# Kernel optimization log

Measured on AMD Instinct MI355X. Metric: run time of the kernel, lower is better.

## Reference

```python
import jax, jax.numpy as jnp
import numpy as np

N_QUBITS = 10
N_LAYERS = 2
B = 4096
D_IN = 512
D_OUT = 256


def _apply_1q(state, gate, wire, n):
    # state: (B, 2**n) complex64; gate: (2,2) shared or (B,2,2) batched
    b = state.shape[0]
    left, right = 2 ** wire, 2 ** (n - wire - 1)
    s = state.reshape(b, left, 2, right)
    if gate.ndim == 3:
        s = jnp.einsum('bij,bljr->blir', gate, s)
    else:
        s = jnp.einsum('ij,bljr->blir', gate, s)
    return s.reshape(b, 2 ** n)


def _apply_cnot(state, c, t, n):
    # CNOT(control=c, target=t): flip target axis on the control=1 slice
    b = state.shape[0]
    a, d = (c, t) if c < t else (t, c)
    s = state.reshape(b, 2 ** a, 2, 2 ** (d - a - 1), 2, 2 ** (n - d - 1))
    if c < t:
        s = s.at[:, :, 1].set(jnp.flip(s[:, :, 1], axis=3))
    else:
        s = s.at[:, :, :, :, 1].set(jnp.flip(s[:, :, :, :, 1], axis=2))
    return s.reshape(b, 2 ** n)


def _quantum_circuit(angles, qweights):
    # AngleEmbedding (RX) + StronglyEntanglingLayers (Rot + ring CNOTs), expval(PauliZ_i)
    b, n = angles.shape
    n_layers = qweights.shape[0]
    state = jnp.zeros((b, 2 ** n), jnp.complex64).at[:, 0].set(1.0)
    # AngleEmbedding default rotation='X': RX(angle_i) on wire i
    half = 0.5 * angles
    cx = jnp.cos(half).astype(jnp.complex64)
    sx = ((-1j) * jnp.sin(half)).astype(jnp.complex64)
    for i in range(n):
        gate = jnp.stack([jnp.stack([cx[:, i], sx[:, i]], -1),
                          jnp.stack([sx[:, i], cx[:, i]], -1)], -2)  # (B,2,2)
        state = _apply_1q(state, gate, i, n)
    for l in range(n_layers):
        phi, theta, omega = qweights[l, :, 0], qweights[l, :, 1], qweights[l, :, 2]
        ct = jnp.cos(0.5 * theta).astype(jnp.complex64)
        st = jnp.sin(0.5 * theta).astype(jnp.complex64)
        epo = jnp.exp(-0.5j * (phi + omega)).astype(jnp.complex64)
        epm = jnp.exp(-0.5j * (phi - omega)).astype(jnp.complex64)
        # Rot(phi,theta,omega) = RZ(omega) RY(theta) RZ(phi)
        gates = jnp.stack([jnp.stack([epo * ct, -jnp.conj(epm) * st], -1),
                           jnp.stack([epm * st, jnp.conj(epo) * ct], -1)], -2)  # (n,2,2)
        for i in range(n):
            state = _apply_1q(state, gates[i], i, n)
        if n > 1:
            r = (l % (n - 1)) + 1  # default StronglyEntanglingLayers range
            for i in range(n):
                state = _apply_cnot(state, i, (i + r) % n, n)
    probs = state.real ** 2 + state.imag ** 2  # (B, 2**n)
    k = np.arange(2 ** n)
    # wire 0 is the most-significant bit; z_i = +1 for bit 0, -1 for bit 1
    zmat = (1 - 2 * ((k[None, :] >> (n - 1 - np.arange(n))[:, None]) & 1)).astype(np.float32)
    return probs @ zmat.T  # (B, n)


def setup_inputs() -> dict:
    key = jax.random.key(0)
    ks = jax.random.split(key, 6)
    x = jax.random.normal(ks[0], (B, D_IN), jnp.float32)
    W_in = jax.random.normal(ks[1], (D_IN, N_QUBITS), jnp.float32) / np.float32(np.sqrt(D_IN))
    b_in = jnp.zeros((N_QUBITS,), jnp.float32)
    qweights = jax.random.uniform(ks[2], (N_LAYERS, N_QUBITS, 3), jnp.float32, 0.0, 2.0 * np.pi)
    W1 = jax.random.normal(ks[3], (N_QUBITS, 64), jnp.float32) / np.float32(np.sqrt(N_QUBITS))
    b1 = jnp.zeros((64,), jnp.float32)
    W2 = jax.random.normal(ks[4], (64, D_OUT), jnp.float32) / np.float32(8.0)
    b2 = jnp.zeros((D_OUT,), jnp.float32)
    return {'x': x, 'W_in': W_in, 'b_in': b_in, 'qweights': qweights,
            'W1': W1, 'b1': b1, 'W2': W2, 'b2': b2}


def reference(x, W_in, b_in, qweights, W1, b1, W2, b2):
    angles = x @ W_in + b_in          # input projection -> rotation angles
    z = _quantum_circuit(angles, qweights)  # (B, n_qubits) PauliZ expvals
    h = jax.nn.relu(z @ W1 + b1)
    return jnp.tanh(h @ W2 + b2)
```

## Files before the change

kernel.cpp:

```cpp
#include <hip/hip_runtime.h>
#include <math.h>

#define NQ 10

__device__ __forceinline__ void write_term(int u, const float abc[NQ][3],
                                           uint2* __restrict__ terms) {
    const int lane = u & 255, s = u >> 8;
    int q = -1, g0 = 0;
    if      (lane < 32)  { q = 8; g0 = 0;   }
    else if (lane < 64)  { q = 9; g0 = 32;  }
    else if (lane < 96)  { q = 0; g0 = 64;  }
    else if (lane < 128) { q = 1; g0 = 96;  }
    else if (lane < 160) { q = 6; g0 = 128; }
    else if (lane < 192) { q = 7; g0 = 160; }
    else if (lane < 200) { q = 4; g0 = 192; }
    else if (lane < 208) { q = 5; g0 = 200; }
    else if (lane < 216) { q = 2; g0 = 208; }
    else if (lane < 224) { q = 3; g0 = 216; }
    if (q < 0) { terms[u] = make_uint2(0u, 0u); return; }
    const int tau = (lane - g0) * 8 + s;

    int m = 1 << q;
    for (int ii = NQ - 1; ii >= 0; --ii) {
        int tt = (ii + 2) % NQ;
        if ((m >> tt) & 1) m ^= 1 << ii;
    }
    const int Lp = __popc(m);
    int cnt = 1;
    for (int k = 0; k < Lp; ++k) cnt *= 3;
    if (tau >= cnt) { terms[u] = make_uint2(0u, 0u); return; }

    int rem = tau;
    unsigned xm = 0, zm = 0;
    float coef = 1.f;
    for (int i = 0; i < NQ; ++i) {
        if ((m >> i) & 1) {
            int d = rem % 3; rem /= 3;
            coef *= abc[i][d];
            if (d == 0)      { xm |= 1u << i; }
            else if (d == 1) { xm |= 1u << i; zm |= 1u << i; }
            else             { zm |= 1u << i; }
        }
    }
    unsigned sgn = 0;
    for (int i = NQ - 1; i >= 0; --i) {
        int c = i, tt = (i + 1) % NQ;
        unsigned xc = (xm >> c) & 1u, zt = (zm >> tt) & 1u;
        unsigned xt = (xm >> tt) & 1u, zc = (zm >> c) & 1u;
        sgn ^= xc & zt & (xt ^ zc ^ 1u);
        xm ^= xc << tt;
        zm ^= zt << c;
    }
    if (sgn) coef = -coef;

    unsigned nib = 0;
    for (int p = 0; p < 5; ++p) {
        unsigned c0 = ((xm >> (2 * p)) & 1u) | (((zm >> (2 * p)) & 1u) << 1);
        unsigned c1 = ((xm >> (2 * p + 1)) & 1u) | (((zm >> (2 * p + 1)) & 1u) << 1);
        nib |= (c0 | (c1 << 2)) << (4 * p);
    }
    terms[u] = make_uint2(nib, __float_as_uint(coef));
}

__global__ __launch_bounds__(1024) void qse_setup(const float* __restrict__ qw,
                                                  uint2* __restrict__ terms,
                                                  float* __restrict__ Rmat) {
    __shared__ float abc[NQ][3];
    const int t = threadIdx.x;
    if (t < NQ) {
        {
            float phi = qw[t * 3 + 0], th = qw[t * 3 + 1], om = qw[t * 3 + 2];
            float st_, ct;  sincosf(0.5f * th, &st_, &ct);
            float spo, cpo; sincosf(0.5f * (phi + om), &spo, &cpo);
            float spm, cpm; sincosf(0.5f * (phi - om), &spm, &cpm);
            Rmat[t * 8 + 0] =  cpo * ct;  Rmat[t * 8 + 1] = -spo * ct;
            Rmat[t * 8 + 2] = -cpm * st_; Rmat[t * 8 + 3] = -spm * st_;
            Rmat[t * 8 + 4] =  cpm * st_; Rmat[t * 8 + 5] = -spm * st_;
            Rmat[t * 8 + 6] =  cpo * ct;  Rmat[t * 8 + 7] =  spo * ct;
        }
        {
            float phi = qw[30 + t * 3 + 0], th = qw[30 + t * 3 + 1], om = qw[30 + t * 3 + 2];
            float st_, ct;  sincosf(0.5f * th, &st_, &ct);
            float spo, cpo; sincosf(0.5f * (phi + om), &spo, &cpo);
            float spm, cpm; sincosf(0.5f * (phi - om), &spm, &cpm);
            float2 G00 = make_float2(cpo * ct, -spo * ct);
            float2 G01 = make_float2(-cpm * st_, -spm * st_);
            float2 G10 = make_float2(cpm * st_, -spm * st_);
            float2 G11 = make_float2(cpo * ct, spo * ct);
            float re = G00.x * G01.x + G00.y * G01.y - (G10.x * G11.x + G10.y * G11.y);
            float im = G00.x * G01.y - G00.y * G01.x - (G10.x * G11.y - G10.y * G11.x);
            float A00 = G00.x * G00.x + G00.y * G00.y - (G10.x * G10.x + G10.y * G10.y);
            float A11 = G01.x * G01.x + G01.y * G01.y - (G11.x * G11.x + G11.y * G11.y);
            abc[t][0] = re;
            abc[t][1] = -im;
            abc[t][2] = 0.5f * (A00 - A11);
        }
    }
    __syncthreads();
    write_term(t, abc, terms);
    write_term(t + 1024, abc, terms);
}

__global__ __launch_bounds__(256) void k_angles(const float* __restrict__ x,
                                                const float* __restrict__ W_in,
                                                const float* __restrict__ b_in,
                                                float* __restrict__ ang) {
    const int t = threadIdx.x, lane = t & 63, wv = t >> 6;
    const int row = blockIdx.x * 4 + wv;
    const float* xr = x + (size_t)row * 512;
    float acc[NQ];
    #pragma unroll
    for (int q = 0; q < NQ; ++q) acc[q] = 0.f;
    for (int k = 0; k < 8; ++k) {
        int j = lane + 64 * k;
        float xv = xr[j];
        const float2* wr = (const float2*)(W_in + j * NQ);
        #pragma unroll
        for (int h = 0; h < 5; ++h) {
            float2 w2 = wr[h];
            acc[2 * h]     = fmaf(xv, w2.x, acc[2 * h]);
            acc[2 * h + 1] = fmaf(xv, w2.y, acc[2 * h + 1]);
        }
    }
    #pragma unroll
    for (int off = 32; off > 0; off >>= 1) {
        #pragma unroll
        for (int q = 0; q < NQ; ++q) acc[q] += __shfl_xor(acc[q], off);
    }
    if (lane == 0) {
        #pragma unroll
        for (int q = 0; q < NQ; ++q) ang[row * NQ + q] = acc[q] + b_in[q];
    }
}

__global__ __launch_bounds__(256) void k_quantum(const float* __restrict__ ang,
                                                 const float* __restrict__ Rmat,
                                                 const uint2* __restrict__ terms,
                                                 float* __restrict__ z) {
    __shared__ float E2d[4][5][32];
    const int t = threadIdx.x;
    const int row0 = blockIdx.x * 4;

    if (t < 80) {
        const int rr = t / 20, rem = t % 20, p = rem >> 2, c1 = rem & 3;
        const int i0 = 2 * p, i1 = i0 + 1;
        float a0 = ang[(row0 + rr) * NQ + i0];
        float a1 = ang[(row0 + rr) * NQ + i1];
        float s0, c0f, s1, c1f;
        sincosf(0.5f * a0, &s0, &c0f);
        sincosf(0.5f * a1, &s1, &c1f);
        const float* Rp0 = Rmat + i0 * 8;
        const float* Rp1 = Rmat + i1 * 8;
        float2 u0 = make_float2(fmaf(Rp0[0], c0f, s0 * Rp0[3]), fmaf(Rp0[1], c0f, -s0 * Rp0[2]));
        float2 u1 = make_float2(fmaf(Rp0[4], c0f, s0 * Rp0[7]), fmaf(Rp0[5], c0f, -s0 * Rp0[6]));
        float ex0 = 2.f * (u0.x * u1.x + u0.y * u1.y);
        float ey0 = 2.f * (u0.x * u1.y - u0.y * u1.x);
        float ez0 = u0.x * u0.x + u0.y * u0.y - u1.x * u1.x - u1.y * u1.y;
        float2 v0 = make_float2(fmaf(Rp1[0], c1f, s1 * Rp1[3]), fmaf(Rp1[1], c1f, -s1 * Rp1[2]));
        float2 v1 = make_float2(fmaf(Rp1[4], c1f, s1 * Rp1[7]), fmaf(Rp1[5], c1f, -s1 * Rp1[6]));
        float ex1 = 2.f * (v0.x * v1.x + v0.y * v1.y);
        float ey1 = 2.f * (v0.x * v1.y - v0.y * v1.x);
        float ez1 = v0.x * v0.x + v0.y * v0.y - v1.x * v1.x - v1.y * v1.y;
        float e1 = (c1 == 0) ? 1.f : (c1 == 1) ? ex1 : (c1 == 2) ? ez1 : ey1;
        float e0arr[4] = {1.f, ex0, ez0, ey0};
        #pragma unroll
        for (int cc = 0; cc < 4; ++cc) {
            float v = e0arr[cc] * e1;
            int idx = cc | (c1 << 2);
            E2d[rr][p][2 * idx]     = v;
            E2d[rr][p][2 * idx + 1] = v;
        }
    }
    __syncthreads();

    float accR[4] = {0.f, 0.f, 0.f, 0.f};
    {
        const float* E2p = &E2d[0][0][0] + (t & 1);
        #pragma unroll
        for (int s = 0; s < 8; ++s) {
            uint2 tms = terms[s * 256 + t];
            const float cf = __uint_as_float(tms.y);
            const unsigned nib = tms.x;
            #pragma unroll
            for (int rr = 0; rr < 4; ++rr) {
                float pr = cf;
                #pragma unroll
                for (int p = 0; p < 5; ++p)
                    pr *= E2p[(rr * 5 + p) * 32 + 2 * ((nib >> (4 * p)) & 15u)];
                accR[rr] += pr;
            }
        }
    }
    #pragma unroll
    for (int rr = 0; rr < 4; ++rr) {
        accR[rr] += __shfl_xor(accR[rr], 1);
        accR[rr] += __shfl_xor(accR[rr], 2);
        accR[rr] += __shfl_xor(accR[rr], 4);
    }
    if (t < 192) {
        #pragma unroll
        for (int rr = 0; rr < 4; ++rr) {
            accR[rr] += __shfl_xor(accR[rr], 8);
            accR[rr] += __shfl_xor(accR[rr], 16);
        }
    }
    int qx = -1;
    if      (t == 0)   qx = 8;
    else if (t == 32)  qx = 9;
    else if (t == 64)  qx = 0;
    else if (t == 96)  qx = 1;
    else if (t == 128) qx = 6;
    else if (t == 160) qx = 7;
    else if (t == 192) qx = 4;
    else if (t == 200) qx = 5;
    else if (t == 208) qx = 2;
    else if (t == 216) qx = 3;
    if (qx >= 0) {
        #pragma unroll
        for (int rr = 0; rr < 4; ++rr) z[(row0 + rr) * NQ + qx] = accR[rr];
    }
}

__global__ __launch_bounds__(256) void k_mlp(const float* __restrict__ z,
                                             const float* __restrict__ W1,
                                             const float* __restrict__ b1,
                                             const float* __restrict__ W2,
                                             const float* __restrict__ b2,
                                             float* __restrict__ out) {
    __shared__ float zsh[8][NQ];
    __shared__ float hsh[8][64];
    const int t = threadIdx.x;
    const int row0 = blockIdx.x * 8;

    if (t < 80) zsh[t / NQ][t % NQ] = z[(row0 + t / NQ) * NQ + t % NQ];
    __syncthreads();

    #pragma unroll
    for (int rep = 0; rep < 2; ++rep) {
        const int job = t + rep * 256;
        const int rr = job >> 6, c = job & 63;
        float a = b1[c];
        #pragma unroll
        for (int i = 0; i < NQ; ++i) a = fmaf(zsh[rr][i], W1[i * 64 + c], a);
        hsh[rr][c] = fmaxf(a, 0.f);
    }
    __syncthreads();

    float oacc[8];
    {
        const float bb = b2[t];
        #pragma unroll
        for (int rr = 0; rr < 8; ++rr) oacc[rr] = bb;
    }
    for (int j4 = 0; j4 < 16; ++j4) {
        const float w0 = W2[(4 * j4 + 0) * 256 + t];
        const float w1 = W2[(4 * j4 + 1) * 256 + t];
        const float w2 = W2[(4 * j4 + 2) * 256 + t];
        const float w3 = W2[(4 * j4 + 3) * 256 + t];
        #pragma unroll
        for (int rr = 0; rr < 8; ++rr) {
            float4 hv = *(const float4*)&hsh[rr][4 * j4];
            oacc[rr] = fmaf(hv.x, w0, oacc[rr]);
            oacc[rr] = fmaf(hv.y, w1, oacc[rr]);
            oacc[rr] = fmaf(hv.z, w2, oacc[rr]);
            oacc[rr] = fmaf(hv.w, w3, oacc[rr]);
        }
    }
    #pragma unroll
    for (int rr = 0; rr < 8; ++rr)
        out[(size_t)(row0 + rr) * 256 + t] = tanhf(oacc[rr]);
}

extern "C" void kernel_launch(void* const* d_in, const int* in_sizes, int n_in,
                              void* d_out, int out_size, void* d_ws, size_t ws_size,
                              hipStream_t stream) {
    const float* x    = (const float*)d_in[0];
    const float* W_in = (const float*)d_in[1];
    const float* b_in = (const float*)d_in[2];
    const float* qw   = (const float*)d_in[3];
    const float* W1   = (const float*)d_in[4];
    const float* b1   = (const float*)d_in[5];
    const float* W2   = (const float*)d_in[6];
    const float* b2   = (const float*)d_in[7];
    float* out = (float*)d_out;

    uint2* terms = (uint2*)d_ws;
    float* Rmat  = (float*)((char*)d_ws + 16384);
    float* ang   = (float*)((char*)d_ws + 32768);
    float* zbuf  = (float*)((char*)d_ws + 196608);

    qse_setup<<<1, 1024, 0, stream>>>(qw, terms, Rmat);
    k_angles <<<1024, 256, 0, stream>>>(x, W_in, b_in, ang);
    k_quantum<<<1024, 256, 0, stream>>>((const float*)ang, (const float*)Rmat,
                                        (const uint2*)terms, zbuf);
    k_mlp    <<<512, 256, 0, stream>>>((const float*)zbuf, W1, b1, W2, b2, out);
}
```

Baseline: 102.5 us.

## Fuse angle projection, circuit evaluation and MLP into one kernel

Merges the angle projection, quantum expectation and MLP kernels into a single per-4-row kernel that passes angles and expectations through shared memory rather than global buffers. It also splits the setup kernel across 8 blocks of 256 threads, vectorises the x loads to float4, and prefetches the term table into registers. tanhf is replaced by an exp-based fast tanh. This removes two launches and global round trips, but the MLP stage now covers 4 rows per block instead of 8, so W2 reuse drops and register pressure rises.

```diff
diff --git a/kernel.cpp b/kernel.cpp
--- a/kernel.cpp
+++ b/kernel.cpp
@@ -62,13 +62,14 @@
     terms[u] = make_uint2(nib, __float_as_uint(coef));
 }
 
-__global__ __launch_bounds__(1024) void qse_setup(const float* __restrict__ qw,
-                                                  uint2* __restrict__ terms,
-                                                  float* __restrict__ Rmat) {
+__global__ __launch_bounds__(256) void qse_setup(const float* __restrict__ qw,
+                                                 uint2* __restrict__ terms,
+                                                 float* __restrict__ Rmat) {
     __shared__ float abc[NQ][3];
     const int t = threadIdx.x;
+    const int b = blockIdx.x;
     if (t < NQ) {
-        {
+        if (b == 0) {
             float phi = qw[t * 3 + 0], th = qw[t * 3 + 1], om = qw[t * 3 + 2];
             float st_, ct;  sincosf(0.5f * th, &st_, &ct);
             float spo, cpo; sincosf(0.5f * (phi + om), &spo, &cpo);
@@ -97,55 +98,92 @@
         }
     }
     __syncthreads();
-    write_term(t, abc, terms);
-    write_term(t + 1024, abc, terms);
-}
-
-__global__ __launch_bounds__(256) void k_angles(const float* __restrict__ x,
-                                                const float* __restrict__ W_in,
-                                                const float* __restrict__ b_in,
-                                                float* __restrict__ ang) {
-    const int t = threadIdx.x, lane = t & 63, wv = t >> 6;
-    const int row = blockIdx.x * 4 + wv;
-    const float* xr = x + (size_t)row * 512;
-    float acc[NQ];
+    write_term(b * 256 + t, abc, terms);
+}
+
+__device__ __forceinline__ float fast_tanh(float v) {
+    float e = __expf(2.f * v);
+    return 1.f - 2.f / (e + 1.f);
+}
+
+__global__ __launch_bounds__(256) void qse_mega(
+    const float* __restrict__ x,
+    const float* __restrict__ W_in,
+    const float* __restrict__ b_in,
+    const float* __restrict__ W1,
+    const float* __restrict__ b1,
+    const float* __restrict__ W2,
+    const float* __restrict__ b2,
+    const uint2* __restrict__ terms,
+    const float* __restrict__ Rmat,
+    float* __restrict__ out)
+{
+    __shared__ float angsh[4][NQ];
+    __shared__ float E2d[4][5][32];
+    __shared__ float zsh[4][NQ];
+    __shared__ float hsh[4][64];
+
+    const int t = threadIdx.x;
+    const int lane = t & 63;
+    const int wv = t >> 6;
+    const int row0 = blockIdx.x * 4;
+
+    uint2 tm[8];
     #pragma unroll
-    for (int q = 0; q < NQ; ++q) acc[q] = 0.f;
-    for (int k = 0; k < 8; ++k) {
-        int j = lane + 64 * k;
-        float xv = xr[j];
-        const float2* wr = (const float2*)(W_in + j * NQ);
-        #pragma unroll
-        for (int h = 0; h < 5; ++h) {
-            float2 w2 = wr[h];
-            acc[2 * h]     = fmaf(xv, w2.x, acc[2 * h]);
-            acc[2 * h + 1] = fmaf(xv, w2.y, acc[2 * h + 1]);
-        }
-    }
-    #pragma unroll
-    for (int off = 32; off > 0; off >>= 1) {
-        #pragma unroll
-        for (int q = 0; q < NQ; ++q) acc[q] += __shfl_xor(acc[q], off);
-    }
-    if (lane == 0) {
-        #pragma unroll
-        for (int q = 0; q < NQ; ++q) ang[row * NQ + q] = acc[q] + b_in[q];
-    }
-}
-
-__global__ __launch_bounds__(256) void k_quantum(const float* __restrict__ ang,
-                                                 const float* __restrict__ Rmat,
-                                                 const uint2* __restrict__ terms,
-                                                 float* __restrict__ z) {
-    __shared__ float E2d[4][5][32];
-    const int t = threadIdx.x;
-    const int row0 = blockIdx.x * 4;
+    for (int s = 0; s < 8; ++s) tm[s] = terms[s * 256 + t];
+
+    {
+        float acc[NQ];
+        #pragma unroll
+        for (int q = 0; q < NQ; ++q) acc[q] = 0.f;
+        const float4* xr4 = (const float4*)(x + (size_t)(row0 + wv) * 512);
+        #pragma unroll
+        for (int k = 0; k < 2; ++k) {
+            const int j4 = lane + 64 * k;
+            const float4 xv = xr4[j4];
+            const float* wr = W_in + (4 * j4) * NQ;
+            #pragma unroll
+            for (int h = 0; h < 5; ++h) {
+                float2 w2 = ((const float2*)wr)[h];
+                acc[2*h]   = fmaf(xv.x, w2.x, acc[2*h]);
+                acc[2*h+1] = fmaf(xv.x, w2.y, acc[2*h+1]);
+            }
+            #pragma unroll
+            for (int h = 0; h < 5; ++h) {
+                float2 w2 = ((const float2*)(wr + NQ))[h];
+                acc[2*h]   = fmaf(xv.y, w2.x, acc[2*h]);
+                acc[2*h+1] = fmaf(xv.y, w2.y, acc[2*h+1]);
+            }
+            #pragma unroll
+            for (int h = 0; h < 5; ++h) {
+                float2 w2 = ((const float2*)(wr + 2 * NQ))[h];
+                acc[2*h]   = fmaf(xv.z, w2.x, acc[2*h]);
+                acc[2*h+1] = fmaf(xv.z, w2.y, acc[2*h+1]);
+            }
+            #pragma unroll
+            for (int h = 0; h < 5; ++h) {
+                float2 w2 = ((const float2*)(wr + 3 * NQ))[h];
+                acc[2*h]   = fmaf(xv.w, w2.x, acc[2*h]);
+                acc[2*h+1] = fmaf(xv.w, w2.y, acc[2*h+1]);
+            }
+        }
+        #pragma unroll
+        for (int off = 32; off > 0; off >>= 1) {
+            #pragma unroll
+            for (int q = 0; q < NQ; ++q) acc[q] += __shfl_xor(acc[q], off);
+        }
+        if (lane == 0) {
+            #pragma unroll
+            for (int q = 0; q < NQ; ++q) angsh[wv][q] = acc[q] + b_in[q];
+        }
+    }
+    __syncthreads();
 
     if (t < 80) {
         const int rr = t / 20, rem = t % 20, p = rem >> 2, c1 = rem & 3;
         const int i0 = 2 * p, i1 = i0 + 1;
-        float a0 = ang[(row0 + rr) * NQ + i0];
-        float a1 = ang[(row0 + rr) * NQ + i1];
+        float a0 = angsh[rr][i0];
+        float a1 = angsh[rr][i1];
         float s0, c0f, s1, c1f;
         sincosf(0.5f * a0, &s0, &c0f);
         sincosf(0.5f * a1, &s1, &c1f);
@@ -178,9 +216,8 @@
         const float* E2p = &E2d[0][0][0] + (t & 1);
         #pragma unroll
         for (int s = 0; s < 8; ++s) {
-            uint2 tms = terms[s * 256 + t];
-            const float cf = __uint_as_float(tms.y);
-            const unsigned nib = tms.x;
+            const float cf = __uint_as_float(tm[s].y);
+            const unsigned nib = tm[s].x;
             #pragma unroll
             for (int rr = 0; rr < 4; ++rr) {
                 float pr = cf;
@@ -204,41 +241,27 @@
             accR[rr] += __shfl_xor(accR[rr], 16);
         }
     }
-    int qx = -1;
-    if      (t == 0)   qx = 8;
-    else if (t == 32)  qx = 9;
-    else if (t == 64)  qx = 0;
-    else if (t == 96)  qx = 1;
-    else if (t == 128) qx = 6;
-    else if (t == 160) qx = 7;
-    else if (t == 192) qx = 4;
-    else if (t == 200) qx = 5;
-    else if (t == 208) qx = 2;
-    else if (t == 216) qx = 3;
-    if (qx >= 0) {
-        #pragma unroll
-        for (int rr = 0; rr < 4; ++rr) z[(row0 + rr) * NQ + qx] = accR[rr];
-    }
-}
-
-__global__ __launch_bounds__(256) void k_mlp(const float* __restrict__ z,
-                                             const float* __restrict__ W1,
-                                             const float* __restrict__ b1,
-                                             const float* __restrict__ W2,
-                                             const float* __restrict__ b2,
-                                             float* __restrict__ out) {
-    __shared__ float zsh[8][NQ];
-    __shared__ float hsh[8][64];
-    const int t = threadIdx.x;
-    const int row0 = blockIdx.x * 8;
-
-    if (t < 80) zsh[t / NQ][t % NQ] = z[(row0 + t / NQ) * NQ + t % NQ];
-    __syncthreads();
-
-    #pragma unroll
-    for (int rep = 0; rep < 2; ++rep) {
-        const int job = t + rep * 256;
-        const int rr = job >> 6, c = job & 63;
+    {
+        int qx = -1;
+        if      (t == 0)   qx = 8;
+        else if (t == 32)  qx = 9;
+        else if (t == 64)  qx = 0;
+        else if (t == 96)  qx = 1;
+        else if (t == 128) qx = 6;
+        else if (t == 160) qx = 7;
+        else if (t == 192) qx = 4;
+        else if (t == 200) qx = 5;
+        else if (t == 208) qx = 2;
+        else if (t == 216) qx = 3;
+        if (qx >= 0) {
+            #pragma unroll
+            for (int rr = 0; rr < 4; ++rr) zsh[rr][qx] = accR[rr];
+        }
+    }
+    __syncthreads();
+
+    {
+        const int rr = t >> 6, c = t & 63;
         float a = b1[c];
         #pragma unroll
         for (int i = 0; i < NQ; ++i) a = fmaf(zsh[rr][i], W1[i * 64 + c], a);
@@ -246,29 +269,29 @@
     }
     __syncthreads();
 
-    float oacc[8];
-    {
+    {
+        float oacc[4];
         const float bb = b2[t];
         #pragma unroll
-        for (int rr = 0; rr < 8; ++rr) oacc[rr] = bb;
-    }
-    for (int j4 = 0; j4 < 16; ++j4) {
-        const float w0 = W2[(4 * j4 + 0) * 256 + t];
-        const float w1 = W2[(4 * j4 + 1) * 256 + t];
-        const float w2 = W2[(4 * j4 + 2) * 256 + t];
-        const float w3 = W2[(4 * j4 + 3) * 256 + t];
-        #pragma unroll
-        for (int rr = 0; rr < 8; ++rr) {
-            float4 hv = *(const float4*)&hsh[rr][4 * j4];
-            oacc[rr] = fmaf(hv.x, w0, oacc[rr]);
-            oacc[rr] = fmaf(hv.y, w1, oacc[rr]);
-            oacc[rr] = fmaf(hv.z, w2, oacc[rr]);
-            oacc[rr] = fmaf(hv.w, w3, oacc[rr]);
-        }
-    }
-    #pragma unroll
-    for (int rr = 0; rr < 8; ++rr)
-        out[(size_t)(row0 + rr) * 256 + t] = tanhf(oacc[rr]);
+        for (int rr = 0; rr < 4; ++rr) oacc[rr] = bb;
+        for (int j4 = 0; j4 < 16; ++j4) {
+            const float w0 = W2[(4 * j4 + 0) * 256 + t];
+            const float w1 = W2[(4 * j4 + 1) * 256 + t];
+            const float w2 = W2[(4 * j4 + 2) * 256 + t];
+            const float w3 = W2[(4 * j4 + 3) * 256 + t];
+            #pragma unroll
+            for (int rr = 0; rr < 4; ++rr) {
+                float4 hv = *(const float4*)&hsh[rr][4 * j4];
+                oacc[rr] = fmaf(hv.x, w0, oacc[rr]);
+                oacc[rr] = fmaf(hv.y, w1, oacc[rr]);
+                oacc[rr] = fmaf(hv.z, w2, oacc[rr]);
+                oacc[rr] = fmaf(hv.w, w3, oacc[rr]);
+            }
+        }
+        #pragma unroll
+        for (int rr = 0; rr < 4; ++rr)
+            out[(size_t)(row0 + rr) * 256 + t] = fast_tanh(oacc[rr]);
+    }
 }
 
 extern "C" void kernel_launch(void* const* d_in, const int* in_sizes, int n_in,
@@ -286,12 +309,8 @@
 
     uint2* terms = (uint2*)d_ws;
     float* Rmat  = (float*)((char*)d_ws + 16384);
-    float* ang   = (float*)((char*)d_ws + 32768);
-    float* zbuf  = (float*)((char*)d_ws + 196608);
-
-    qse_setup<<<1, 1024, 0, stream>>>(qw, terms, Rmat);
-    k_angles <<<1024, 256, 0, stream>>>(x, W_in, b_in, ang);
-    k_quantum<<<1024, 256, 0, stream>>>((const float*)ang, (const float*)Rmat,
-                                        (const uint2*)terms, zbuf);
-    k_mlp    <<<512, 256, 0, stream>>>((const float*)zbuf, W1, b1, W2, b2, out);
-}
+
+    qse_setup<<<8, 256, 0, stream>>>(qw, terms, Rmat);
+    qse_mega<<<1024, 256, 0, stream>>>(x, W_in, b_in, W1, b1, W2, b2,
+                                       (const uint2*)terms, (const float*)Rmat, out);
+}
```

Result: faster. 87.52 us (-14.7%).
